# Kernel tuning notes

Hardware: AMD Instinct MI355X
Metric: run time of the kernel (lower is better)

Reference implementation:

```python
import jax, jax.numpy as jnp
import numpy as np

N, V, F, H, B, HID = 256, 32, 128, 8, 8, 64
R_MAX = 5.0
DH = F // H


def fc_edges(n):
    a = np.arange(n)
    s, r = np.meshgrid(a, a, indexing="ij")
    m = s != r
    return jnp.asarray(s[m]), jnp.asarray(r[m])

SENDERS, RECEIVERS = fc_edges(N)
E = N * (N - 1)


def sph_harmonics(u):
    # u: [..., 3] unit vectors -> [..., 15] = l=1(3)+l=2(5)+l=3(7), e3nn 'component' normalization
    x, y, z = u[..., 0], u[..., 1], u[..., 2]
    s3 = 3.0 ** 0.5; s5 = 5.0 ** 0.5; s7 = 7.0 ** 0.5
    s15 = 15.0 ** 0.5; s105 = 105.0 ** 0.5
    s35_8 = (35.0 / 8.0) ** 0.5; s21_8 = (21.0 / 8.0) ** 0.5
    l1 = [s3 * y, s3 * z, s3 * x]
    l2 = [s15 * x * y, s15 * y * z, 0.5 * s5 * (3 * z * z - 1),
          s15 * x * z, 0.5 * s15 * (x * x - y * y)]
    l3 = [s35_8 * y * (3 * x * x - y * y), s105 * x * y * z,
          s21_8 * y * (5 * z * z - 1), 0.5 * s7 * z * (5 * z * z - 3),
          s21_8 * x * (5 * z * z - 1), 0.5 * s105 * z * (x * x - y * y),
          s35_8 * x * (x * x - 3 * y * y)]
    return jnp.stack(l1 + l2 + l3, axis=-1)


def radial_embed(lengths):
    # Bessel basis (e3nn.bessel) times soft envelope (e3nn.soft_envelope)
    x = jnp.maximum(lengths, 1e-6)[..., None]
    k = jnp.arange(1, B + 1, dtype=lengths.dtype)
    bes = (2.0 / R_MAX) ** 0.5 * jnp.sin(k * jnp.pi * x / R_MAX) / x
    def sus(t):
        return jnp.where(t > 0, jnp.exp(-1.0 / jnp.where(t > 0, t, 1.0)), 0.0)
    env = 1.2 * sus(2.0 * (1.0 - lengths / R_MAX)) / sus(jnp.asarray(2.0))
    return bes * env[..., None]


def setup_inputs():
    key = jax.random.key(0)
    ks = jax.random.split(key, 16)
    def w(k, shape):
        return jax.random.normal(k, shape, jnp.float32) / (shape[0] ** 0.5)
    D_edge = 2 * F + V * B
    return {
        "positions": jax.random.normal(ks[0], (N, V, 3), jnp.float32),
        "features": jax.random.normal(ks[1], (N, F), jnp.float32),
        "We1": w(ks[2], (D_edge, HID)), "be1": jnp.zeros((HID,), jnp.float32),
        "We2": w(ks[3], (HID, HID)), "be2": jnp.zeros((HID,), jnp.float32),
        "W_q": w(ks[4], (F, F)), "W_k": w(ks[5], (HID, F)),
        "W_v": w(ks[6], (F, F)), "W_vec": w(ks[7], (HID, V)),
        "W_mix": w(ks[8], (V, V)),
        "M1": w(ks[9], (F, HID)), "bm1": jnp.zeros((HID,), jnp.float32),
        "M2": w(ks[10], (HID, HID)), "bm2": jnp.zeros((HID,), jnp.float32),
        "M3": w(ks[11], (HID, F)), "bm3": jnp.zeros((F,), jnp.float32),
    }


def reference(positions, features, We1, be1, We2, be2, W_q, W_k, W_v, W_vec,
              W_mix, M1, bm1, M2, bm2, M3, bm3):
    act = jax.nn.selu
    s, r = SENDERS, RECEIVERS
    vectors = positions[s] - positions[r]                        # [E, V, 3]
    lengths = jnp.sqrt(jnp.sum(vectors * vectors, -1) + 1e-18)   # [E, V] safe_norm
    unit = vectors / lengths[..., None]
    sph = sph_harmonics(unit)                                    # [E, V, 15]
    radial = radial_embed(lengths).reshape(E, V * B)             # [E, V*B]
    edge_weight_cutoff = jnp.ones((E,), positions.dtype)

    # edge MLP on invariants (radial embedding + src/dst scalar features)
    edge_in = jnp.concatenate([features[s], features[r], radial], -1)
    h = act(edge_in @ We1 + be1)
    h = act(h @ We2 + be2)                                       # [E, HID]

    # multi-head attention over incoming edges per node (segment softmax)
    q = (features @ W_q).reshape(N, H, DH)
    k = (h @ W_k).reshape(E, H, DH)
    logit = jnp.einsum("ehd,ehd->eh", k, q[r]) / (DH ** 0.5)
    lmax = jax.ops.segment_max(logit, r, num_segments=N)
    ex = edge_weight_cutoff[:, None] * jnp.exp(logit - lmax[r])
    denom = jax.ops.segment_sum(ex, r, num_segments=N)
    alpha = ex / (denom[r] + 1e-12)                              # [E, H]

    # invariant (0e) values
    v = (features[s] @ W_v).reshape(E, H, DH)
    inv_agg = jax.ops.segment_sum(alpha[..., None] * v, r, num_segments=N).reshape(N, F)

    # equivariant (1o) values: scalar-gated l=1 spherical harmonics (sqrt(3)*unit)
    coeff = h @ W_vec                                            # [E, V]
    alpha_v = jnp.repeat(alpha, V // H, axis=1)                  # [E, V]
    vec_msg = ((alpha_v * coeff) * (3.0 ** 0.5))[..., None] * unit  # [E, V, 3]
    vec_agg = jax.ops.segment_sum(vec_msg, r, num_segments=N)    # [N, V, 3]
    vec_out = jnp.einsum("nvc,vw->nwc", vec_agg, W_mix)

    # final invariant MLP + residuals
    hi = act(inv_agg @ M1 + bm1)
    hi = act(hi @ M2 + bm2)
    inv_out = hi @ M3 + bm3
    return (vec_out + positions, inv_out + features)
```

## Files before the change

kernel.cpp:

```cpp
#include <hip/hip_runtime.h>
#include <hip/hip_bf16.h>

#define NN 256
#define VC 32
#define FD 128

typedef unsigned int uint32;
typedef unsigned short u16;
typedef __attribute__((ext_vector_type(8))) short bf16x8;
typedef __attribute__((ext_vector_type(4))) float f32x4;

__device__ __forceinline__ float selu_f(float x) {
    const float lam = 1.0507009873554805f;
    const float la  = 1.7580993408473766f;
    return x > 0.f ? lam * x : la * (__expf(x) - 1.f);
}

__device__ __forceinline__ u16 f32_to_bf16_rne(float f) {
    uint32 u = __float_as_uint(f);
    uint32 r = (u + 0x7fffu + ((u >> 16) & 1u)) >> 16;
    return (u16)r;
}

__device__ __forceinline__ float bf16_to_f32(u16 h) {
    return __uint_as_float(((uint32)h) << 16);
}

__global__ __launch_bounds__(256) void k1_pre(
    const float* __restrict__ feat, const float* __restrict__ We1,
    const float* __restrict__ be1, const float* __restrict__ Wq,
    const float* __restrict__ Wk, const float* __restrict__ Wv,
    const float* __restrict__ Wvec, const float* __restrict__ We2,
    const float* __restrict__ pos,
    float* __restrict__ A, float* __restrict__ Bf, u16* __restrict__ kqb,
    u16* __restrict__ w1b, u16* __restrict__ we2b, u16* __restrict__ wvb,
    u16* __restrict__ fvtH, u16* __restrict__ fvtL,
    u16* __restrict__ ptH, u16* __restrict__ ptL,
    float* __restrict__ lgg2, u16* __restrict__ cfg2)
{
    __shared__ float fl[FD];
    __shared__ float ql[FD];
    const int n = blockIdx.x;
    const int t = threadIdx.x;
    {
        const int gid = n*256 + t;
        if (gid < 16384) {
            const int c = gid >> 8, k = gid & 255;
            w1b[gid] = f32_to_bf16_rne(We1[(256 + k)*64 + c]);
        } else if (gid < 20480) {
            const int o = gid - 16384;
            const int c = o >> 6, k = o & 63;
            we2b[o] = f32_to_bf16_rne(We2[k*64 + c]);
        } else if (gid < 22528) {
            const int o = gid - 20480;
            const int v = o >> 6, k = o & 63;
            wvb[o] = f32_to_bf16_rne(Wvec[k*32 + v]);
        }
    }
    if (t < FD) fl[t] = feat[n*FD + t];
    __syncthreads();
    if (t < 64) {
        float a = 0.f;
        for (int i = 0; i < FD; ++i) a = fmaf(fl[i], We1[i*64 + t], a);
        A[n*64 + t] = a;
    } else if (t < 128) {
        const int j = t - 64;
        float a = be1[j];
        for (int i = 0; i < FD; ++i) a = fmaf(fl[i], We1[(FD+i)*64 + j], a);
        Bf[n*64 + j] = a;
    } else {
        const int j = t - 128;
        float a = 0.f;
        for (int i = 0; i < FD; ++i) a = fmaf(fl[i], Wq[i*FD + j], a);
        ql[j] = a * 0.25f;
    }
    if (t < FD) {
        float a = 0.f;
        for (int i = 0; i < FD; ++i) a = fmaf(fl[i], Wv[i*FD + t], a);
        const u16 hi = f32_to_bf16_rne(a);
        const u16 lo = f32_to_bf16_rne(a - bf16_to_f32(hi));
        fvtH[t*256 + n] = hi;
        fvtL[t*256 + n] = lo;
    }
    if (t < 128) {
        const int v = t >> 2, c = t & 3;
        const float val = (c < 3) ? pos[(n*VC + v)*3 + c] : 1.0f;
        const u16 hi = f32_to_bf16_rne(val);
        const u16 lo = f32_to_bf16_rne(val - bf16_to_f32(hi));
        ptH[(v*4+c)*256 + n] = hi;
        ptL[(v*4+c)*256 + n] = lo;
    }
    if (t < 8)  lgg2[n*2048 + t*256 + n] = -1e30f;
    if (t < 32) cfg2[n*8192 + t*256 + n] = 0;
    __syncthreads();
    for (int o = t; o < 512; o += 256) {
        const int h = o >> 6, j = o & 63;
        float a = 0.f;
        #pragma unroll
        for (int d = 0; d < 16; ++d)
            a = fmaf(Wk[j*FD + h*16 + d], ql[h*16 + d], a);
        kqb[n*512 + o] = f32_to_bf16_rne(a);
    }
}

__global__ __launch_bounds__(256) void k2_edge(
    const float* __restrict__ pos, const float* __restrict__ be2,
    const float* __restrict__ Ag, const float* __restrict__ Bfg,
    const u16* __restrict__ w1b, const u16* __restrict__ we2b,
    const u16* __restrict__ wvb, const u16* __restrict__ kqb,
    float* __restrict__ lgg2, u16* __restrict__ cfg2)
{
    __shared__ u16 rad[8192];
    __shared__ u16 h1b[32*64];
    __shared__ u16 h2b[32*64];
    __shared__ float invl[32*33];

    const int t = threadIdx.x;
    const int wave = t >> 6, l = t & 63;
    const int li = l & 15, q = l >> 4;
    const int mh = wave >> 1, eh = wave & 1;
    const int r = blockIdx.x >> 1, tpart = blockIdx.x & 1;
    const int e = eh*16 + li;
    const int swz16 = (e & 7) << 3;

    bf16x8 w1A[2][8];
    #pragma unroll
    for (int mt = 0; mt < 2; ++mt) {
        const int c = mh*32 + mt*16 + li;
        #pragma unroll
        for (int kb = 0; kb < 8; ++kb)
            w1A[mt][kb] = *(const bf16x8*)(w1b + c*256 + kb*32 + q*8);
    }
    bf16x8 we2A[2][2];
    #pragma unroll
    for (int mt = 0; mt < 2; ++mt) {
        const int c2 = mh*32 + mt*16 + li;
        #pragma unroll
        for (int kb = 0; kb < 2; ++kb)
            we2A[mt][kb] = *(const bf16x8*)(we2b + c2*64 + kb*32 + q*8);
    }
    bf16x8 wvA[2];
    {
        const int v = mh*16 + li;
        #pragma unroll
        for (int kb = 0; kb < 2; ++kb)
            wvA[kb] = *(const bf16x8*)(wvb + v*64 + kb*32 + q*8);
    }
    bf16x8 kqA[2];
    if (li < 8) {
        #pragma unroll
        for (int kb = 0; kb < 2; ++kb)
            kqA[kb] = *(const bf16x8*)(kqb + r*512 + li*64 + kb*32 + q*8);
    } else {
        #pragma unroll
        for (int kb = 0; kb < 2; ++kb)
            #pragma unroll
            for (int j = 0; j < 8; ++j) kqA[kb][j] = 0;
    }
    float bfreg[2][4], be2reg[2][4];
    #pragma unroll
    for (int mt = 0; mt < 2; ++mt)
        #pragma unroll
        for (int rg = 0; rg < 4; ++rg) {
            const int c = mh*32 + mt*16 + q*4 + rg;
            bfreg[mt][rg] = Bfg[r*64 + c];
            be2reg[mt][rg] = be2[c];
        }

    for (int it = 0; it < 4; ++it) {
        const int s0 = (tpart*4 + it) * 32;
        const int sp = s0 + e;
        int s = sp + (sp >= r ? 1 : 0); if (s > 255) s = 255;
        __syncthreads();

        float As[2][4];
        #pragma unroll
        for (int mt = 0; mt < 2; ++mt)
            #pragma unroll
            for (int rg = 0; rg < 4; ++rg)
                As[mt][rg] = Ag[s*64 + mh*32 + mt*16 + q*4 + rg];

        {
            const int ep = t & 31, vg = t >> 5;
            const int spp = s0 + ep;
            int sv = spp + (spp >= r ? 1 : 0); if (sv > 255) sv = 255;
            #pragma unroll
            for (int kk = 0; kk < 4; ++kk) {
                const int v = vg*4 + kk;
                const float* ps = pos + (sv*VC + v)*3;
                const float* pr = pos + (r*VC + v)*3;
                const float dx = ps[0]-pr[0], dy = ps[1]-pr[1], dz = ps[2]-pr[2];
                const float d2 = fmaf(dx,dx,fmaf(dy,dy,dz*dz)) + 1e-18f;
                const float len = sqrtf(d2);
                invl[ep*33 + v] = rsqrtf(d2);
                const float x = fmaxf(len, 1e-6f);
                const float tt2 = 2.f - 0.4f*len;
                const float env = tt2 > 0.f ? 1.9784655248401538f * __expf(-1.f/tt2) : 0.f;
                const float coefc = 0.6324555320336759f * env / x;
                float s_cur, c1;
                __sincosf(0.6283185307179586f * x, &s_cur, &c1);
                const float c2x = 2.f * c1;
                float s_prev = 0.f;
                union { uint4 u4; u16 us[8]; } pk;
                #pragma unroll
                for (int b = 0; b < 8; ++b) {
                    pk.us[b] = f32_to_bf16_rne(coefc * s_cur);
                    const float s_next = fmaf(c2x, s_cur, -s_prev);
                    s_prev = s_cur; s_cur = s_next;
                }
                *(uint4*)((char*)rad + ((ep*512 + v*16) ^ ((ep & 15) << 4))) = pk.u4;
            }
        }
        __syncthreads();

        f32x4 d1[2] = {{0.f,0.f,0.f,0.f},{0.f,0.f,0.f,0.f}};
        #pragma unroll
        for (int kb = 0; kb < 8; ++kb) {
            const bf16x8 rf = *(const bf16x8*)((const char*)rad +
                                ((e*512 + (kb*4+q)*16) ^ ((e & 15) << 4)));
            d1[0] = __builtin_amdgcn_mfma_f32_16x16x32_bf16(w1A[0][kb], rf, d1[0], 0, 0, 0);
            d1[1] = __builtin_amdgcn_mfma_f32_16x16x32_bf16(w1A[1][kb], rf, d1[1], 0, 0, 0);
        }
        #pragma unroll
        for (int mt = 0; mt < 2; ++mt) {
            const int c0 = mh*32 + mt*16 + q*4;
            const u16 p0 = f32_to_bf16_rne(selu_f(d1[mt][0] + As[mt][0] + bfreg[mt][0]));
            const u16 p1 = f32_to_bf16_rne(selu_f(d1[mt][1] + As[mt][1] + bfreg[mt][1]));
            const u16 p2 = f32_to_bf16_rne(selu_f(d1[mt][2] + As[mt][2] + bfreg[mt][2]));
            const u16 p3 = f32_to_bf16_rne(selu_f(d1[mt][3] + As[mt][3] + bfreg[mt][3]));
            *(uint32*)&h1b[e*64 + ((c0)     ^ swz16)] = (uint32)p0 | ((uint32)p1 << 16);
            *(uint32*)&h1b[e*64 + ((c0 + 2) ^ swz16)] = (uint32)p2 | ((uint32)p3 << 16);
        }
        __syncthreads();

        f32x4 d2[2] = {{0.f,0.f,0.f,0.f},{0.f,0.f,0.f,0.f}};
        #pragma unroll
        for (int kb = 0; kb < 2; ++kb) {
            const bf16x8 hb = *(const bf16x8*)&h1b[e*64 + ((kb*32 + q*8) ^ swz16)];
            d2[0] = __builtin_amdgcn_mfma_f32_16x16x32_bf16(we2A[0][kb], hb, d2[0], 0, 0, 0);
            d2[1] = __builtin_amdgcn_mfma_f32_16x16x32_bf16(we2A[1][kb], hb, d2[1], 0, 0, 0);
        }
        #pragma unroll
        for (int mt = 0; mt < 2; ++mt) {
            const int c0 = mh*32 + mt*16 + q*4;
            const u16 p0 = f32_to_bf16_rne(selu_f(d2[mt][0] + be2reg[mt][0]));
            const u16 p1 = f32_to_bf16_rne(selu_f(d2[mt][1] + be2reg[mt][1]));
            const u16 p2 = f32_to_bf16_rne(selu_f(d2[mt][2] + be2reg[mt][2]));
            const u16 p3 = f32_to_bf16_rne(selu_f(d2[mt][3] + be2reg[mt][3]));
            *(uint32*)&h2b[e*64 + ((c0)     ^ swz16)] = (uint32)p0 | ((uint32)p1 << 16);
            *(uint32*)&h2b[e*64 + ((c0 + 2) ^ swz16)] = (uint32)p2 | ((uint32)p3 << 16);
        }
        __syncthreads();

        f32x4 d3 = {0.f,0.f,0.f,0.f};
        f32x4 dl = {0.f,0.f,0.f,0.f};
        #pragma unroll
        for (int kb = 0; kb < 2; ++kb) {
            const bf16x8 hb = *(const bf16x8*)&h2b[e*64 + ((kb*32 + q*8) ^ swz16)];
            d3 = __builtin_amdgcn_mfma_f32_16x16x32_bf16(wvA[kb], hb, d3, 0, 0, 0);
            if (mh == 0)
                dl = __builtin_amdgcn_mfma_f32_16x16x32_bf16(kqA[kb], hb, dl, 0, 0, 0);
        }
        if (sp < 255) {
            #pragma unroll
            for (int rg = 0; rg < 4; ++rg) {
                const int v = mh*16 + q*4 + rg;
                cfg2[(size_t)r*8192 + v*256 + s] =
                    f32_to_bf16_rne(d3[rg] * 1.7320508075688772f * invl[e*33 + v]);
            }
            if (mh == 0 && q < 2) {
                #pragma unroll
                for (int rg = 0; rg < 4; ++rg)
                    lgg2[(size_t)r*2048 + (q*4+rg)*256 + s] = dl[rg];
            }
        }
    }
}

__global__ __launch_bounds__(64) void k3b_agg(
    const float* __restrict__ lgg2, const u16* __restrict__ cfg2,
    const u16* __restrict__ fvtH, const u16* __restrict__ fvtL,
    const u16* __restrict__ ptH, const u16* __restrict__ ptL,
    float* __restrict__ inv, float* __restrict__ vec4)
{
    const int l = threadIdx.x, li = l & 15, q = l >> 4;
    const int b = blockIdx.x;
    if (b < 128) {
        const int h = b >> 4, r0 = (b & 15) * 16;
        bf16x8 fH[8], fL[8];
        #pragma unroll
        for (int kb = 0; kb < 8; ++kb) {
            fH[kb] = *(const bf16x8*)(fvtH + (h*16+li)*256 + kb*32 + q*8);
            fL[kb] = *(const bf16x8*)(fvtL + (h*16+li)*256 + kb*32 + q*8);
        }
        const float* lgr = lgg2 + (size_t)(r0+li)*2048 + h*256;
        float mx = -3.0e38f;
        #pragma unroll
        for (int kb = 0; kb < 8; ++kb) {
            const float4 g0 = *(const float4*)(lgr + kb*32 + q*8);
            const float4 g1 = *(const float4*)(lgr + kb*32 + q*8 + 4);
            mx = fmaxf(mx, fmaxf(fmaxf(g0.x,g0.y), fmaxf(g0.z,g0.w)));
            mx = fmaxf(mx, fmaxf(fmaxf(g1.x,g1.y), fmaxf(g1.z,g1.w)));
        }
        mx = fmaxf(mx, __shfl_xor(mx, 16));
        mx = fmaxf(mx, __shfl_xor(mx, 32));
        float sm = 0.f;
        f32x4 C = {0.f,0.f,0.f,0.f};
        #pragma unroll
        for (int kb = 0; kb < 8; ++kb) {
            const float4 g0 = *(const float4*)(lgr + kb*32 + q*8);
            const float4 g1 = *(const float4*)(lgr + kb*32 + q*8 + 4);
            float ev[8];
            ev[0]=__expf(g0.x-mx); ev[1]=__expf(g0.y-mx); ev[2]=__expf(g0.z-mx); ev[3]=__expf(g0.w-mx);
            ev[4]=__expf(g1.x-mx); ev[5]=__expf(g1.y-mx); ev[6]=__expf(g1.z-mx); ev[7]=__expf(g1.w-mx);
            bf16x8 a;
            #pragma unroll
            for (int j = 0; j < 8; ++j) { sm += ev[j]; a[j] = (short)f32_to_bf16_rne(ev[j]); }
            C = __builtin_amdgcn_mfma_f32_16x16x32_bf16(a, fH[kb], C, 0, 0, 0);
            C = __builtin_amdgcn_mfma_f32_16x16x32_bf16(a, fL[kb], C, 0, 0, 0);
        }
        sm += __shfl_xor(sm, 16);
        sm += __shfl_xor(sm, 32);
        #pragma unroll
        for (int rg = 0; rg < 4; ++rg) {
            const float d = __shfl(sm, q*4 + rg);
            inv[(r0 + q*4 + rg)*128 + h*16 + li] = C[rg] / (d + 1e-12f);
        }
    } else {
        const int b2 = b - 128, v = b2 >> 4, r0 = (b2 & 15) * 16;
        const int h = v >> 2;
        bf16x8 pH[8], pL[8];
        #pragma unroll
        for (int kb = 0; kb < 8; ++kb) {
            if (li < 4) {
                pH[kb] = *(const bf16x8*)(ptH + (v*4+li)*256 + kb*32 + q*8);
                pL[kb] = *(const bf16x8*)(ptL + (v*4+li)*256 + kb*32 + q*8);
            } else {
                #pragma unroll
                for (int j = 0; j < 8; ++j) { pH[kb][j] = 0; pL[kb][j] = 0; }
            }
        }
        const float* lgr = lgg2 + (size_t)(r0+li)*2048 + h*256;
        const u16*  cfr = cfg2 + (size_t)(r0+li)*8192 + v*256;
        float mx = -3.0e38f;
        #pragma unroll
        for (int kb = 0; kb < 8; ++kb) {
            const float4 g0 = *(const float4*)(lgr + kb*32 + q*8);
            const float4 g1 = *(const float4*)(lgr + kb*32 + q*8 + 4);
            mx = fmaxf(mx, fmaxf(fmaxf(g0.x,g0.y), fmaxf(g0.z,g0.w)));
            mx = fmaxf(mx, fmaxf(fmaxf(g1.x,g1.y), fmaxf(g1.z,g1.w)));
        }
        mx = fmaxf(mx, __shfl_xor(mx, 16));
        mx = fmaxf(mx, __shfl_xor(mx, 32));
        float sm = 0.f;
        f32x4 C = {0.f,0.f,0.f,0.f};
        #pragma unroll
        for (int kb = 0; kb < 8; ++kb) {
            const float4 g0 = *(const float4*)(lgr + kb*32 + q*8);
            const float4 g1 = *(const float4*)(lgr + kb*32 + q*8 + 4);
            const bf16x8 cf8 = *(const bf16x8*)(cfr + kb*32 + q*8);
            float ev[8];
            ev[0]=__expf(g0.x-mx); ev[1]=__expf(g0.y-mx); ev[2]=__expf(g0.z-mx); ev[3]=__expf(g0.w-mx);
            ev[4]=__expf(g1.x-mx); ev[5]=__expf(g1.y-mx); ev[6]=__expf(g1.z-mx); ev[7]=__expf(g1.w-mx);
            bf16x8 a;
            #pragma unroll
            for (int j = 0; j < 8; ++j) {
                sm += ev[j];
                a[j] = (short)f32_to_bf16_rne(ev[j] * bf16_to_f32((u16)cf8[j]));
            }
            C = __builtin_amdgcn_mfma_f32_16x16x32_bf16(a, pH[kb], C, 0, 0, 0);
            C = __builtin_amdgcn_mfma_f32_16x16x32_bf16(a, pL[kb], C, 0, 0, 0);
        }
        sm += __shfl_xor(sm, 16);
        sm += __shfl_xor(sm, 32);
        #pragma unroll
        for (int rg = 0; rg < 4; ++rg) {
            const float d = __shfl(sm, q*4 + rg);
            if (li < 4)
                vec4[(r0 + q*4 + rg)*128 + v*4 + li] = C[rg] / (d + 1e-12f);
        }
    }
}

__global__ __launch_bounds__(256) void k3c_out(
    const float* __restrict__ pos, const float* __restrict__ feat,
    const float* __restrict__ inv, const float* __restrict__ vec4,
    const float* __restrict__ Wmix,
    const float* __restrict__ M1, const float* __restrict__ bm1,
    const float* __restrict__ M2, const float* __restrict__ bm2,
    const float* __restrict__ M3, const float* __restrict__ bm3,
    float* __restrict__ out0, float* __restrict__ out1)
{
    __shared__ float m1s[128*64];
    __shared__ float m2s[64*64];
    __shared__ float m3s[64*128];
    __shared__ float wmixs[32*32];
    __shared__ float invas[4*128];
    __shared__ float vec4s[4*128];
    __shared__ float pos4[4*96];
    __shared__ float vecls[4*96];
    __shared__ float hi1s[4*64];
    __shared__ float hi2s[4*64];
    __shared__ float b1s[64], b2s[64], b3s[128];
    const int t = threadIdx.x;
    const int r0 = blockIdx.x * 4;
    for (int o = t; o < 8192; o += 256) m1s[o] = M1[o];
    for (int o = t; o < 4096; o += 256) m2s[o] = M2[o];
    for (int o = t; o < 8192; o += 256) m3s[o] = M3[o];
    for (int o = t; o < 1024; o += 256) wmixs[o] = Wmix[o];
    for (int o = t; o < 512; o += 256) invas[o] = inv[r0*128 + o];
    for (int o = t; o < 512; o += 256) vec4s[o] = vec4[r0*128 + o];
    for (int o = t; o < 384; o += 256) pos4[o] = pos[r0*96 + o];
    if (t < 64) { b1s[t] = bm1[t]; b2s[t] = bm2[t]; }
    if (t < 128) b3s[t] = bm3[t];
    __syncthreads();
    for (int o = t; o < 384; o += 256) {
        const int rr = o / 96, j = o - rr*96;
        const int v = j / 3, c = j - v*3;
        vecls[o] = vec4s[rr*128 + v*4 + c] - vec4s[rr*128 + v*4 + 3] * pos4[o];
    }
    __syncthreads();
    {
        const int f = t & 63, rr = t >> 6;
        float acc = b1s[f];
        #pragma unroll 8
        for (int k = 0; k < 128; ++k)
            acc = fmaf(invas[rr*128 + k], m1s[k*64 + f], acc);
        hi1s[rr*64 + f] = selu_f(acc);
    }
    __syncthreads();
    {
        const int f = t & 63, rr = t >> 6;
        float acc = b2s[f];
        #pragma unroll 8
        for (int k = 0; k < 64; ++k)
            acc = fmaf(hi1s[rr*64 + k], m2s[k*64 + f], acc);
        hi2s[rr*64 + f] = selu_f(acc);
    }
    __syncthreads();
    for (int o = t; o < 512; o += 256) {
        const int f = o & 127, rr = o >> 7;
        float acc = b3s[f];
        #pragma unroll 8
        for (int k = 0; k < 64; ++k)
            acc = fmaf(hi2s[rr*64 + k], m3s[k*128 + f], acc);
        out1[(r0+rr)*128 + f] = acc + feat[(r0+rr)*128 + f];
    }
    for (int o = t; o < 384; o += 256) {
        const int rr = o / 96, j = o - rr*96;
        const int w = j / 3, c = j - w*3;
        float acc = 0.f;
        #pragma unroll
        for (int v = 0; v < 32; ++v)
            acc = fmaf(vecls[rr*96 + v*3 + c], wmixs[v*32 + w], acc);
        out0[(r0+rr)*96 + j] = acc + pos4[o];
    }
}

extern "C" void kernel_launch(void* const* d_in, const int* in_sizes, int n_in,
                              void* d_out, int out_size, void* d_ws, size_t ws_size,
                              hipStream_t stream)
{
    const float* pos  = (const float*)d_in[0];
    const float* feat = (const float*)d_in[1];
    const float* We1  = (const float*)d_in[2];
    const float* be1  = (const float*)d_in[3];
    const float* We2  = (const float*)d_in[4];
    const float* be2  = (const float*)d_in[5];
    const float* Wq   = (const float*)d_in[6];
    const float* Wk   = (const float*)d_in[7];
    const float* Wv   = (const float*)d_in[8];
    const float* Wvec = (const float*)d_in[9];
    const float* Wmix = (const float*)d_in[10];
    const float* M1   = (const float*)d_in[11];
    const float* bm1  = (const float*)d_in[12];
    const float* M2   = (const float*)d_in[13];
    const float* bm2  = (const float*)d_in[14];
    const float* M3   = (const float*)d_in[15];
    const float* bm3  = (const float*)d_in[16];

    char* ws = (char*)d_ws;
    float* A    = (float*)(ws + 0);
    float* Bf   = (float*)(ws + 65536);
    u16*   kqb  = (u16*)(ws + 131072);
    u16*   w1b  = (u16*)(ws + 393216);
    u16*   we2b = (u16*)(ws + 425984);
    u16*   wvb  = (u16*)(ws + 434176);
    u16*   fvtH = (u16*)(ws + 438272);
    u16*   fvtL = (u16*)(ws + 503808);
    u16*   ptH  = (u16*)(ws + 569344);
    u16*   ptL  = (u16*)(ws + 634880);
    float* lgg2 = (float*)(ws + 700416);
    u16*   cfg2 = (u16*)(ws + 2797568);
    float* inv   = (float*)(ws + 0);
    float* vec4  = (float*)(ws + 131072);
    if (ws_size < (size_t)6991872) return;

    float* out0 = (float*)d_out;
    float* out1 = out0 + NN*VC*3;

    hipLaunchKernelGGL(k1_pre, dim3(256), dim3(256), 0, stream,
                       feat, We1, be1, Wq, Wk, Wv, Wvec, We2, pos,
                       A, Bf, kqb, w1b, we2b, wvb, fvtH, fvtL, ptH, ptL, lgg2, cfg2);
    hipLaunchKernelGGL(k2_edge, dim3(512), dim3(256), 0, stream,
                       pos, be2, A, Bf, w1b, we2b, wvb, kqb, lgg2, cfg2);
    hipLaunchKernelGGL(k3b_agg, dim3(640), dim3(64), 0, stream,
                       lgg2, cfg2, fvtH, fvtL, ptH, ptL, inv, vec4);
    hipLaunchKernelGGL(k3c_out, dim3(64), dim3(256), 0, stream,
                       pos, feat, inv, vec4, Wmix,
                       M1, bm1, M2, bm2, M3, bm3, out0, out1);
}
```

Baseline: 50.24 us.

## Split edge kernel finer, dual MFMA accumulators, per-node output MLP kernel

The edge kernel now launches four blocks per receiver instead of two, each handling two 32-sender chunks instead of four, to raise parallelism and occupancy on the GPU. The aggregation kernel splits the hi/lo MFMA chain into two independent accumulators so consecutive MFMAs no longer depend on each other. The final output kernel switches from 64 blocks of 256 threads that stage all MLP weights in LDS to 256 single-wave blocks that read weights straight from global/cache, removing the large LDS staging cost. The trade-off is that the per-block weight preload in the edge kernel is repeated across twice as many blocks, and weight reads in the output kernel repeat across more blocks.

Result: slower. 53.73 us (+7.0%).

```diff
diff --git a/kernel.cpp b/kernel.cpp
--- a/kernel.cpp
+++ b/kernel.cpp
@@ -119,7 +119,7 @@
     const int wave = t >> 6, l = t & 63;
     const int li = l & 15, q = l >> 4;
     const int mh = wave >> 1, eh = wave & 1;
-    const int r = blockIdx.x >> 1, tpart = blockIdx.x & 1;
+    const int r = blockIdx.x >> 2, part = blockIdx.x & 3;
     const int e = eh*16 + li;
     const int swz16 = (e & 7) << 3;
 
@@ -167,8 +167,8 @@
             be2reg[mt][rg] = be2[c];
         }
 
-    for (int it = 0; it < 4; ++it) {
-        const int s0 = (tpart*4 + it) * 32;
+    for (int it = 0; it < 2; ++it) {
+        const int s0 = (part*2 + it) * 32;
         const int sp = s0 + e;
         int s = sp + (sp >= r ? 1 : 0); if (s > 255) s = 255;
         __syncthreads();
@@ -305,7 +305,8 @@
         mx = fmaxf(mx, __shfl_xor(mx, 16));
         mx = fmaxf(mx, __shfl_xor(mx, 32));
         float sm = 0.f;
-        f32x4 C = {0.f,0.f,0.f,0.f};
+        f32x4 Ch = {0.f,0.f,0.f,0.f};
+        f32x4 Cl = {0.f,0.f,0.f,0.f};
         #pragma unroll
         for (int kb = 0; kb < 8; ++kb) {
             const float4 g0 = *(const float4*)(lgr + kb*32 + q*8);
@@ -316,15 +317,15 @@
             bf16x8 a;
             #pragma unroll
             for (int j = 0; j < 8; ++j) { sm += ev[j]; a[j] = (short)f32_to_bf16_rne(ev[j]); }
-            C = __builtin_amdgcn_mfma_f32_16x16x32_bf16(a, fH[kb], C, 0, 0, 0);
-            C = __builtin_amdgcn_mfma_f32_16x16x32_bf16(a, fL[kb], C, 0, 0, 0);
+            Ch = __builtin_amdgcn_mfma_f32_16x16x32_bf16(a, fH[kb], Ch, 0, 0, 0);
+            Cl = __builtin_amdgcn_mfma_f32_16x16x32_bf16(a, fL[kb], Cl, 0, 0, 0);
         }
         sm += __shfl_xor(sm, 16);
         sm += __shfl_xor(sm, 32);
         #pragma unroll
         for (int rg = 0; rg < 4; ++rg) {
             const float d = __shfl(sm, q*4 + rg);
-            inv[(r0 + q*4 + rg)*128 + h*16 + li] = C[rg] / (d + 1e-12f);
+            inv[(r0 + q*4 + rg)*128 + h*16 + li] = (Ch[rg] + Cl[rg]) / (d + 1e-12f);
         }
     } else {
         const int b2 = b - 128, v = b2 >> 4, r0 = (b2 & 15) * 16;
@@ -353,7 +354,8 @@
         mx = fmaxf(mx, __shfl_xor(mx, 16));
         mx = fmaxf(mx, __shfl_xor(mx, 32));
         float sm = 0.f;
-        f32x4 C = {0.f,0.f,0.f,0.f};
+        f32x4 Ch = {0.f,0.f,0.f,0.f};
+        f32x4 Cl = {0.f,0.f,0.f,0.f};
         #pragma unroll
         for (int kb = 0; kb < 8; ++kb) {
             const float4 g0 = *(const float4*)(lgr + kb*32 + q*8);
@@ -368,8 +370,8 @@
                 sm += ev[j];
                 a[j] = (short)f32_to_bf16_rne(ev[j] * bf16_to_f32((u16)cf8[j]));
             }
-            C = __builtin_amdgcn_mfma_f32_16x16x32_bf16(a, pH[kb], C, 0, 0, 0);
-            C = __builtin_amdgcn_mfma_f32_16x16x32_bf16(a, pL[kb], C, 0, 0, 0);
+            Ch = __builtin_amdgcn_mfma_f32_16x16x32_bf16(a, pH[kb], Ch, 0, 0, 0);
+            Cl = __builtin_amdgcn_mfma_f32_16x16x32_bf16(a, pL[kb], Cl, 0, 0, 0);
         }
         sm += __shfl_xor(sm, 16);
         sm += __shfl_xor(sm, 32);
@@ -377,12 +379,12 @@
         for (int rg = 0; rg < 4; ++rg) {
             const float d = __shfl(sm, q*4 + rg);
             if (li < 4)
-                vec4[(r0 + q*4 + rg)*128 + v*4 + li] = C[rg] / (d + 1e-12f);
-        }
-    }
-}
-
-__global__ __launch_bounds__(256) void k3c_out(
+                vec4[(r0 + q*4 + rg)*128 + v*4 + li] = (Ch[rg] + Cl[rg]) / (d + 1e-12f);
+        }
+    }
+}
+
+__global__ __launch_bounds__(64) void k3c_out(
     const float* __restrict__ pos, const float* __restrict__ feat,
     const float* __restrict__ inv, const float* __restrict__ vec4,
     const float* __restrict__ Wmix,
@@ -391,69 +393,49 @@
     const float* __restrict__ M3, const float* __restrict__ bm3,
     float* __restrict__ out0, float* __restrict__ out1)
 {
-    __shared__ float m1s[128*64];
-    __shared__ float m2s[64*64];
-    __shared__ float m3s[64*128];
-    __shared__ float wmixs[32*32];
-    __shared__ float invas[4*128];
-    __shared__ float vec4s[4*128];
-    __shared__ float pos4[4*96];
-    __shared__ float vecls[4*96];
-    __shared__ float hi1s[4*64];
-    __shared__ float hi2s[4*64];
-    __shared__ float b1s[64], b2s[64], b3s[128];
-    const int t = threadIdx.x;
-    const int r0 = blockIdx.x * 4;
-    for (int o = t; o < 8192; o += 256) m1s[o] = M1[o];
-    for (int o = t; o < 4096; o += 256) m2s[o] = M2[o];
-    for (int o = t; o < 8192; o += 256) m3s[o] = M3[o];
-    for (int o = t; o < 1024; o += 256) wmixs[o] = Wmix[o];
-    for (int o = t; o < 512; o += 256) invas[o] = inv[r0*128 + o];
-    for (int o = t; o < 512; o += 256) vec4s[o] = vec4[r0*128 + o];
-    for (int o = t; o < 384; o += 256) pos4[o] = pos[r0*96 + o];
-    if (t < 64) { b1s[t] = bm1[t]; b2s[t] = bm2[t]; }
-    if (t < 128) b3s[t] = bm3[t];
+    __shared__ float inva[128];
+    __shared__ float vec4s[128];
+    __shared__ float pos96[96];
+    __shared__ float vecl[96];
+    __shared__ float hi1[64];
+    __shared__ float hi2[64];
+    const int r = blockIdx.x;
+    const int l = threadIdx.x;
+    inva[l]       = inv[r*128 + l];
+    inva[64 + l]  = inv[r*128 + 64 + l];
+    vec4s[l]      = vec4[r*128 + l];
+    vec4s[64 + l] = vec4[r*128 + 64 + l];
+    for (int o = l; o < 96; o += 64) pos96[o] = pos[r*96 + o];
     __syncthreads();
-    for (int o = t; o < 384; o += 256) {
-        const int rr = o / 96, j = o - rr*96;
-        const int v = j / 3, c = j - v*3;
-        vecls[o] = vec4s[rr*128 + v*4 + c] - vec4s[rr*128 + v*4 + 3] * pos4[o];
-    }
+    for (int o = l; o < 96; o += 64) {
+        const int v = o / 3, c = o - v*3;
+        vecl[o] = vec4s[v*4 + c] - vec4s[v*4 + 3] * pos96[o];
+    }
+    float a1 = bm1[l];
+    #pragma unroll 8
+    for (int k = 0; k < 128; ++k) a1 = fmaf(inva[k], M1[k*64 + l], a1);
+    hi1[l] = selu_f(a1);
     __syncthreads();
-    {
-        const int f = t & 63, rr = t >> 6;
-        float acc = b1s[f];
+    float a2 = bm2[l];
+    #pragma unroll 8
+    for (int k = 0; k < 64; ++k) a2 = fmaf(hi1[k], M2[k*64 + l], a2);
+    hi2[l] = selu_f(a2);
+    __syncthreads();
+    #pragma unroll
+    for (int o0 = 0; o0 < 128; o0 += 64) {
+        const int o = o0 + l;
+        float a = bm3[o];
         #pragma unroll 8
-        for (int k = 0; k < 128; ++k)
-            acc = fmaf(invas[rr*128 + k], m1s[k*64 + f], acc);
-        hi1s[rr*64 + f] = selu_f(acc);
-    }
-    __syncthreads();
-    {
-        const int f = t & 63, rr = t >> 6;
-        float acc = b2s[f];
-        #pragma unroll 8
-        for (int k = 0; k < 64; ++k)
-            acc = fmaf(hi1s[rr*64 + k], m2s[k*64 + f], acc);
-        hi2s[rr*64 + f] = selu_f(acc);
-    }
-    __syncthreads();
-    for (int o = t; o < 512; o += 256) {
-        const int f = o & 127, rr = o >> 7;
-        float acc = b3s[f];
-        #pragma unroll 8
-        for (int k = 0; k < 64; ++k)
-            acc = fmaf(hi2s[rr*64 + k], m3s[k*128 + f], acc);
-        out1[(r0+rr)*128 + f] = acc + feat[(r0+rr)*128 + f];
-    }
-    for (int o = t; o < 384; o += 256) {
-        const int rr = o / 96, j = o - rr*96;
-        const int w = j / 3, c = j - w*3;
-        float acc = 0.f;
+        for (int k = 0; k < 64; ++k) a = fmaf(hi2[k], M3[k*128 + o], a);
+        out1[r*128 + o] = a + feat[r*128 + o];
+    }
+    for (int o = l; o < 96; o += 64) {
+        const int w = o / 3, c = o - w*3;
+        float a = 0.f;
         #pragma unroll
         for (int v = 0; v < 32; ++v)
-            acc = fmaf(vecls[rr*96 + v*3 + c], wmixs[v*32 + w], acc);
-        out0[(r0+rr)*96 + j] = acc + pos4[o];
+            a = fmaf(vecl[v*3 + c], Wmix[v*32 + w], a);
+        out0[r*96 + o] = a + pos96[o];
     }
 }
 
@@ -502,11 +484,11 @@
     hipLaunchKernelGGL(k1_pre, dim3(256), dim3(256), 0, stream,
                        feat, We1, be1, Wq, Wk, Wv, Wvec, We2, pos,
                        A, Bf, kqb, w1b, we2b, wvb, fvtH, fvtL, ptH, ptL, lgg2, cfg2);
-    hipLaunchKernelGGL(k2_edge, dim3(512), dim3(256), 0, stream,
+    hipLaunchKernelGGL(k2_edge, dim3(1024), dim3(256), 0, stream,
                        pos, be2, A, Bf, w1b, we2b, wvb, kqb, lgg2, cfg2);
     hipLaunchKernelGGL(k3b_agg, dim3(640), dim3(64), 0, stream,
                        lgg2, cfg2, fvtH, fvtL, ptH, ptL, inv, vec4);
-    hipLaunchKernelGGL(k3c_out, dim3(64), dim3(256), 0, stream,
+    hipLaunchKernelGGL(k3c_out, dim3(256), dim3(64), 0, stream,
                        pos, feat, inv, vec4, Wmix,
                        M1, bm1, M2, bm2, M3, bm3, out0, out1);
 }
```
